# Kernel optimization log

Hardware: AMD Instinct MI355X
Metric: run time of the kernel (lower is better)

## Reference

```python
import jax, jax.numpy as jnp
import numpy as np

N = 7        # num_nodes
H = 128      # hidden_dim
F_IN = 32    # input_dim
LN_EPS = 1e-5
ALPHA = 0.2  # leaky relu slope
NEG = -9e15  # masking constant from torch code


def _layernorm(x, g, b):
    m = jnp.mean(x, axis=-1, keepdims=True)
    v = jnp.var(x, axis=-1, keepdims=True)
    return (x - m) * jax.lax.rsqrt(v + LN_EPS) * g + b


def setup_inputs() -> dict:
    key = jax.random.key(0)
    ks = jax.random.split(key, 12)
    B, T = 32, 512
    x = jax.random.normal(ks[0], (B, T, F_IN), dtype=jnp.float32)
    adj = jnp.ones((N, N), dtype=jnp.float32)
    # xavier-uniform style init scales (values don't matter for correctness test)
    def xav(k, shape, gain=1.414):
        fan_in, fan_out = shape[0], shape[-1]
        a = gain * np.sqrt(6.0 / (fan_in + fan_out))
        return jax.random.uniform(k, shape, jnp.float32, -a, a)
    Wp = xav(ks[1], (F_IN, N * H), gain=1.0)
    bp = jnp.zeros((N * H,), jnp.float32)
    W1 = xav(ks[2], (H, H))
    a1 = xav(ks[3], (2 * H, 1))
    g1 = jnp.ones((H,), jnp.float32)
    b1 = jnp.zeros((H,), jnp.float32)
    W2 = xav(ks[4], (H, H))
    a2 = xav(ks[5], (2 * H, 1))
    g2 = jnp.ones((H,), jnp.float32)
    b2 = jnp.zeros((H,), jnp.float32)
    return {"x": x, "adj": adj, "Wp": Wp, "bp": bp,
            "W1": W1, "a1": a1, "g1": g1, "b1": b1,
            "W2": W2, "a2": a2, "g2": g2, "b2": b2}


def reference(x, adj, Wp, bp, W1, a1, g1, b1, W2, a2, g2, b2):
    B, T, F = x.shape
    BT = B * T
    # input projection: (B*T, F) -> (B*T, N, H)
    h = (x.reshape(BT, F) @ Wp + bp).reshape(BT, N, H)
    scale = H ** (-0.5)
    mask = adj > 0  # (N, N)
    for (W, a, g, b) in ((W1, a1, g1, b1), (W2, a2, g2, b2)):
        res = h
        Wh = h @ W                               # (BT, N, H)
        # e_ij = leakyrelu(Wh_i . a[:H] + Wh_j . a[H:]) * scale
        f_src = Wh @ a[:H, 0]                    # (BT, N)
        f_dst = Wh @ a[H:, 0]                    # (BT, N)
        e = jax.nn.leaky_relu(f_src[:, :, None] + f_dst[:, None, :], ALPHA) * scale
        e = jnp.where(mask[None, :, :], e, NEG)
        att = jax.nn.softmax(e, axis=2)          # (BT, N, N)
        h_prime = att @ Wh                       # (BT, N, H), concat=False -> no elu
        h = _layernorm(h_prime, g, b) + res
    out = h.mean(axis=1)                         # mean over nodes
    return out.reshape(B, T, H)
```

## Files before the change

kernel.cpp:

```cpp
#include <hip/hip_runtime.h>
#include <math.h>
#include <stdint.h>

#define NN 7
#define HD 128
#define FIN 32
#define TPB 16
#define RPW 28
#define LN_EPS 1e-5f
#define ALPHA 0.2f
#define NEG_CONST -9e15f
#define SCALE 0.08838834764831845f

typedef __bf16 bf16x8 __attribute__((ext_vector_type(8)));
typedef float  f32x4  __attribute__((ext_vector_type(4)));

#define FENCE() do { asm volatile("s_waitcnt lgkmcnt(0)" ::: "memory"); \
                     __builtin_amdgcn_sched_barrier(0); } while (0)

__device__ __forceinline__ uint16_t f2bf_u(float f) {
    union { float f; uint32_t u; } v; v.f = f;
    uint32_t r = v.u + 0x7FFFu + ((v.u >> 16) & 1u);
    return (uint16_t)(r >> 16);
}
__device__ __forceinline__ uint32_t pack2(float a, float b) {
    return (uint32_t)f2bf_u(a) | ((uint32_t)f2bf_u(b) << 16);
}

template <int CTRL>
__device__ __forceinline__ float dpp_add(float v) {
    union { float f; int i; } a, r;
    a.f = v;
    r.i = __builtin_amdgcn_update_dpp(a.i, a.i, CTRL, 0xF, 0xF, false);
    return v + r.f;
}
__device__ __forceinline__ float sum16(float v) {
    v = dpp_add<0xB1>(v);
    v = dpp_add<0x4E>(v);
    v = dpp_add<0x124>(v);
    v = dpp_add<0x128>(v);
    return v;
}

#define WS_W1T  57344
#define WS_W2T  90112
#define WS_VAB  122880
#define WS_BPP  124928
#define WS_GBP  128512

__global__ __launch_bounds__(256) void prep_weights(
    const float* __restrict__ Wp, const float* __restrict__ bp,
    const float* __restrict__ W1, const float* __restrict__ a1,
    const float* __restrict__ g1, const float* __restrict__ b1,
    const float* __restrict__ W2, const float* __restrict__ a2,
    const float* __restrict__ g2, const float* __restrict__ b2,
    uint16_t* __restrict__ WpT, uint16_t* __restrict__ W1T,
    uint16_t* __restrict__ W2T, float* __restrict__ vab,
    float* __restrict__ bpp, float* __restrict__ gbp)
{
    const int bid = blockIdx.x, tid = threadIdx.x;
    if (bid < 112) {
        int idx = bid * 256 + tid;
        int gc = idx >> 5, f = idx & 31;
        int gcp = (gc & ~127) | (((gc & 15) << 3) | ((gc & 127) >> 4));
        WpT[gcp * 32 + f] = f2bf_u(Wp[(size_t)f * (NN * HD) + gc]);
    } else if (bid < 176) {
        int idx = (bid - 112) * 256 + tid;
        int c = idx >> 7, k = idx & 127;
        int kp = ((k & 15) << 3) | (k >> 4);
        W1T[c * 128 + kp] = f2bf_u(W1[(size_t)k * HD + c]);
    } else if (bid < 240) {
        int idx = (bid - 176) * 256 + tid;
        int c = idx >> 7, k = idx & 127;
        int kp = ((k & 15) << 3) | (k >> 4);
        W2T[c * 128 + kp] = f2bf_u(W2[(size_t)k * HD + c]);
    } else {
        for (int d = tid; d < 512; d += 256) {
            int l = d >> 8, which = (d >> 7) & 1, j = d & 127;
            const float* W = l ? W2 : W1;
            const float* a = (l ? a2 : a1) + which * HD;
            const float* row = W + (size_t)j * HD;
            float acc = 0.f;
            #pragma unroll 8
            for (int o = 0; o < HD; o += 4) {
                f32x4 wv = *reinterpret_cast<const f32x4*>(&row[o]);
                acc += wv[0]*a[o] + wv[1]*a[o+1] + wv[2]*a[o+2] + wv[3]*a[o+3];
            }
            int jp = ((j & 15) << 3) | (j >> 4);
            vab[l * 256 + which * 128 + jp] = acc;
        }
        for (int gc = tid; gc < NN * HD; gc += 256) {
            int gcp = (gc & ~127) | (((gc & 15) << 3) | ((gc & 127) >> 4));
            bpp[gcp] = bp[gc];
        }
        for (int e = tid; e < 512; e += 256) {
            int l = e >> 8, which = (e >> 7) & 1, c = e & 127;
            const float* src = l ? (which ? b2 : g2) : (which ? b1 : g1);
            int cp = ((c & 15) << 3) | (c >> 4);
            gbp[l * 256 + which * 128 + cp] = src[c];
        }
    }
}

__global__ __launch_bounds__(256, 2) void gat_fused(
    const float* __restrict__ x, const float* __restrict__ adj,
    const float* __restrict__ bpp,
    const uint16_t* __restrict__ WpT, const uint16_t* __restrict__ W1T,
    const uint16_t* __restrict__ W2T, const float* __restrict__ vab,
    const float* __restrict__ gbp,
    float* __restrict__ out, int BT)
{
    __shared__ __align__(16) float h_s[4][RPW][132];

    const int tid  = threadIdx.x;
    const int lane = tid & 63;
    const int wave = tid >> 6;
    const int frow = lane & 15;
    const int kgrp = lane >> 4;
    const int kb   = kgrp * 8;
    const int t0   = blockIdx.x * TPB;

    const int row0 = (frow > 13) ? 13 : frow;
    const int tb   = (row0 >= NN) ? 1 : 0;
    const int np   = row0 - tb * NN;

    uint32_t amask = 0;
    #pragma unroll
    for (int j = 0; j < NN; ++j)
        amask |= (adj[np * NN + j] > 0.f) ? (1u << j) : 0u;

    bf16x8 bx;
    {
        union { bf16x8 v; uint32_t u[4]; } bu;
        bu.u[0] = bu.u[1] = bu.u[2] = bu.u[3] = 0;
        int tok = t0 + frow;
        if (tok < BT) {
            f32x4 xa = *reinterpret_cast<const f32x4*>(&x[(size_t)tok * FIN + kb]);
            f32x4 xb = *reinterpret_cast<const f32x4*>(&x[(size_t)tok * FIN + kb + 4]);
            bu.u[0] = pack2(xa[0], xa[1]);
            bu.u[1] = pack2(xa[2], xa[3]);
            bu.u[2] = pack2(xb[0], xb[1]);
            bu.u[3] = pack2(xb[2], xb[3]);
        }
        bx = bu.v;
    }

    #pragma unroll 2
    for (int i = 0; i < 14; ++i) {
        int tile = wave * 14 + i;
        bf16x8 av = *reinterpret_cast<const bf16x8*>(WpT + (size_t)(tile * 16 + frow) * FIN + kb);
        f32x4 acc = {0.f, 0.f, 0.f, 0.f};
        acc = __builtin_amdgcn_mfma_f32_16x16x32_bf16(av, bx, acc, 0, 0, 0);
        int tok = t0 + frow;
        if (tok < BT) {
            int gc0 = tile * 16 + kgrp * 4;
            f32x4 bias = *reinterpret_cast<const f32x4*>(&bpp[gc0]);
            f32x4 v = acc + bias;
            int n = gc0 >> 7, kk = gc0 & 127;
            *reinterpret_cast<f32x4*>(&h_s[frow >> 2][(frow & 3) * NN + n][kk]) = v;
        }
    }
    __syncthreads();

    for (int l = 0; l < 2; ++l) {
        const uint16_t* __restrict__ WT  = l ? W2T : W1T;
        const float*    __restrict__ vv0 = vab + l * 256;
        const float*    __restrict__ ggp = gbp + l * 256;

        float facc;
        {
            int which = lane >> 5;
            int rr = lane & 31; if (rr > RPW - 1) rr = RPW - 1;
            const float* hr = &h_s[wave][rr][0];
            const f32x4* vp = reinterpret_cast<const f32x4*>(vv0 + which * HD);
            f32x4 a0 = {0,0,0,0}, a1 = {0,0,0,0};
            #pragma unroll
            for (int i2 = 0; i2 < 16; ++i2) {
                f32x4 hv0 = *reinterpret_cast<const f32x4*>(hr + i2 * 8);
                f32x4 hv1 = *reinterpret_cast<const f32x4*>(hr + i2 * 8 + 4);
                a0 += hv0 * vp[2 * i2];
                a1 += hv1 * vp[2 * i2 + 1];
            }
            f32x4 a = a0 + a1;
            facc = (a[0] + a[1]) + (a[2] + a[3]);
        }

        float p0[NN], p1[NN];
        {
            float fs0 = __shfl(facc, row0, 64);
            float fs1 = __shfl(facc, 14 + row0, 64);
            float e0[NN], e1[NN];
            float mx0 = -INFINITY, mx1 = -INFINITY;
            #pragma unroll
            for (int j = 0; j < NN; ++j) {
                float fd0 = __shfl(facc, 32 + tb * NN + j, 64);
                float fd1 = __shfl(facc, 32 + 14 + tb * NN + j, 64);
                float v0 = fs0 + fd0, v1 = fs1 + fd1;
                v0 = (v0 > 0.f ? v0 : ALPHA * v0) * SCALE;
                v1 = (v1 > 0.f ? v1 : ALPHA * v1) * SCALE;
                bool ok = (amask >> j) & 1u;
                v0 = ok ? v0 : NEG_CONST;
                v1 = ok ? v1 : NEG_CONST;
                e0[j] = v0; mx0 = fmaxf(mx0, v0);
                e1[j] = v1; mx1 = fmaxf(mx1, v1);
            }
            float s0 = 0.f, s1 = 0.f;
            #pragma unroll
            for (int j = 0; j < NN; ++j) {
                e0[j] = __expf(e0[j] - mx0); s0 += e0[j];
                e1[j] = __expf(e1[j] - mx1); s1 += e1[j];
            }
            float i0 = 1.f / s0, i1 = 1.f / s1;
            #pragma unroll
            for (int j = 0; j < NN; ++j) { p0[j] = e0[j] * i0; p1[j] = e1[j] * i1; }
        }

        bf16x8 avA[4], avB[4];
        #pragma unroll
        for (int ks = 0; ks < 4; ++ks) {
            f32x4 ga0 = {0,0,0,0}, ga1 = {0,0,0,0};
            f32x4 gb0 = {0,0,0,0}, gb1 = {0,0,0,0};
            #pragma unroll
            for (int j = 0; j < NN; ++j) {
                const float* hj = &h_s[wave][tb * NN + j][ks * 32 + kb];
                f32x4 h0 = *reinterpret_cast<const f32x4*>(hj);
                f32x4 h1 = *reinterpret_cast<const f32x4*>(hj + 4);
                float pj = p0[j];
                ga0 += h0 * pj;
                ga1 += h1 * pj;
            }
            #pragma unroll
            for (int j = 0; j < NN; ++j) {
                const float* hj = &h_s[wave][14 + tb * NN + j][ks * 32 + kb];
                f32x4 h0 = *reinterpret_cast<const f32x4*>(hj);
                f32x4 h1 = *reinterpret_cast<const f32x4*>(hj + 4);
                float pj = p1[j];
                gb0 += h0 * pj;
                gb1 += h1 * pj;
            }
            union { bf16x8 v; uint32_t u[4]; } ba, bb;
            ba.u[0] = pack2(ga0[0], ga0[1]); ba.u[1] = pack2(ga0[2], ga0[3]);
            ba.u[2] = pack2(ga1[0], ga1[1]); ba.u[3] = pack2(ga1[2], ga1[3]);
            bb.u[0] = pack2(gb0[0], gb0[1]); bb.u[1] = pack2(gb0[2], gb0[3]);
            bb.u[2] = pack2(gb1[0], gb1[1]); bb.u[3] = pack2(gb1[2], gb1[3]);
            avA[ks] = ba.v; avB[ks] = bb.v;
        }

        f32x4 C0[8], C1[8];
        #pragma unroll
        for (int ntl = 0; ntl < 8; ++ntl) {
            const uint16_t* bpg = WT + (size_t)(ntl * 16 + frow) * HD + kb;
            bf16x8 bv0 = *reinterpret_cast<const bf16x8*>(bpg);
            bf16x8 bv1 = *reinterpret_cast<const bf16x8*>(bpg + 32);
            bf16x8 bv2 = *reinterpret_cast<const bf16x8*>(bpg + 64);
            bf16x8 bv3 = *reinterpret_cast<const bf16x8*>(bpg + 96);
            f32x4 a0 = {0,0,0,0}, a1 = {0,0,0,0};
            a0 = __builtin_amdgcn_mfma_f32_16x16x32_bf16(avA[0], bv0, a0, 0, 0, 0);
            a1 = __builtin_amdgcn_mfma_f32_16x16x32_bf16(avB[0], bv0, a1, 0, 0, 0);
            a0 = __builtin_amdgcn_mfma_f32_16x16x32_bf16(avA[1], bv1, a0, 0, 0, 0);
            a1 = __builtin_amdgcn_mfma_f32_16x16x32_bf16(avB[1], bv1, a1, 0, 0, 0);
            a0 = __builtin_amdgcn_mfma_f32_16x16x32_bf16(avA[2], bv2, a0, 0, 0, 0);
            a1 = __builtin_amdgcn_mfma_f32_16x16x32_bf16(avB[2], bv2, a1, 0, 0, 0);
            a0 = __builtin_amdgcn_mfma_f32_16x16x32_bf16(avA[3], bv3, a0, 0, 0, 0);
            a1 = __builtin_amdgcn_mfma_f32_16x16x32_bf16(avB[3], bv3, a1, 0, 0, 0);
            C0[ntl] = a0; C1[ntl] = a1;
        }

        {
            f32x4 gv0 = *reinterpret_cast<const f32x4*>(ggp + frow * 8);
            f32x4 gv1 = *reinterpret_cast<const f32x4*>(ggp + frow * 8 + 4);
            f32x4 bt0 = *reinterpret_cast<const f32x4*>(ggp + 128 + frow * 8);
            f32x4 bt1 = *reinterpret_cast<const f32x4*>(ggp + 128 + frow * 8 + 4);
            #pragma unroll
            for (int tile = 0; tile < 2; ++tile) {
                const f32x4* C = tile ? C1 : C0;
                const int mbase = tile * 14;
                f32x4 s4 = C[0] + C[1];
                f32x4 q4 = C[0]*C[0] + C[1]*C[1];
                #pragma unroll
                for (int nt = 2; nt < 8; ++nt) { s4 += C[nt]; q4 += C[nt]*C[nt]; }
                #pragma unroll
                for (int r = 0; r < 4; ++r) {
                    float s  = sum16(s4[r]);
                    float sq = sum16(q4[r]);
                    float mean = s * (1.f / HD);
                    float var  = sq * (1.f / HD) - mean * mean;
                    float rinv = rsqrtf(var + LN_EPS);
                    int m = kgrp * 4 + r;
                    if (m < 14) {
                        f32x4 coef0 = gv0 * rinv, coef1 = gv1 * rinv;
                        f32x4 off0  = bt0 - coef0 * mean;
                        f32x4 off1  = bt1 - coef1 * mean;
                        float* hp = &h_s[wave][mbase + m][frow * 8];
                        f32x4 h0 = *reinterpret_cast<const f32x4*>(hp) + off0;
                        f32x4 h1 = *reinterpret_cast<const f32x4*>(hp + 4) + off1;
                        h0[0] += C[0][r] * coef0[0];
                        h0[1] += C[1][r] * coef0[1];
                        h0[2] += C[2][r] * coef0[2];
                        h0[3] += C[3][r] * coef0[3];
                        h1[0] += C[4][r] * coef1[0];
                        h1[1] += C[5][r] * coef1[1];
                        h1[2] += C[6][r] * coef1[2];
                        h1[3] += C[7][r] * coef1[3];
                        *reinterpret_cast<f32x4*>(hp)     = h0;
                        *reinterpret_cast<f32x4*>(hp + 4) = h1;
                    }
                }
            }
        }
        FENCE();
    }

    {
        int t_o = lane >> 4;
        int cq  = lane & 15;
        int tok = t0 + wave * 4 + t_o;
        if (tok < BT) {
            f32x4 s0 = {0,0,0,0}, s1 = {0,0,0,0};
            #pragma unroll
            for (int n = 0; n < NN; ++n) {
                const float* hp = &h_s[wave][t_o * NN + n][cq * 8];
                s0 += *reinterpret_cast<const f32x4*>(hp);
                s1 += *reinterpret_cast<const f32x4*>(hp + 4);
            }
            const float inv7 = 1.f / 7.f;
            s0 *= inv7; s1 *= inv7;
            float* ob = out + (size_t)tok * HD;
            ob[0*16+cq] = s0[0]; ob[1*16+cq] = s0[1];
            ob[2*16+cq] = s0[2]; ob[3*16+cq] = s0[3];
            ob[4*16+cq] = s1[0]; ob[5*16+cq] = s1[1];
            ob[6*16+cq] = s1[2]; ob[7*16+cq] = s1[3];
        }
    }
}

extern "C" void kernel_launch(void* const* d_in, const int* in_sizes, int n_in,
                              void* d_out, int out_size, void* d_ws, size_t ws_size,
                              hipStream_t stream) {
    const float* x   = (const float*)d_in[0];
    const float* adj = (const float*)d_in[1];
    const float* Wp  = (const float*)d_in[2];
    const float* bp  = (const float*)d_in[3];
    const float* W1  = (const float*)d_in[4];
    const float* a1  = (const float*)d_in[5];
    const float* g1  = (const float*)d_in[6];
    const float* b1  = (const float*)d_in[7];
    const float* W2  = (const float*)d_in[8];
    const float* a2  = (const float*)d_in[9];
    const float* g2  = (const float*)d_in[10];
    const float* b2  = (const float*)d_in[11];
    const int BT = in_sizes[0] / FIN;
    const int blocks = (BT + TPB - 1) / TPB;

    uint8_t* ws = (uint8_t*)d_ws;
    uint16_t* WpT = (uint16_t*)(ws);
    uint16_t* W1T = (uint16_t*)(ws + WS_W1T);
    uint16_t* W2T = (uint16_t*)(ws + WS_W2T);
    float*    vab = (float*)   (ws + WS_VAB);
    float*    bpp = (float*)   (ws + WS_BPP);
    float*    gbp = (float*)   (ws + WS_GBP);

    prep_weights<<<dim3(241), dim3(256), 0, stream>>>(
        Wp, bp, W1, a1, g1, b1, W2, a2, g2, b2, WpT, W1T, W2T, vab, bpp, gbp);
    gat_fused<<<dim3(blocks), dim3(256), 0, stream>>>(
        x, adj, bpp, WpT, W1T, W2T, vab, gbp, (float*)d_out, BT);
}
```

Measured before the change: 74.86 us.

## Store hidden state in LDS as bf16 and raise occupancy target to 4 blocks

The per-block shared hidden-state buffer changes from fp32 to packed bf16, with unpack helpers at every read and bf16 packing at every write, including the residual/LayerNorm update. This halves LDS footprint and LDS read bandwidth per row, and the launch bound is raised from 2 to 4 blocks per CU to use the freed LDS for more resident waves. The cost is extra pack/unpack ALU work, bf16 rounding of the residual stream across both layers (an accuracy risk), and tighter register limits that may cause spills.

```diff
diff --git a/kernel.cpp b/kernel.cpp
--- a/kernel.cpp
+++ b/kernel.cpp
@@ -25,6 +25,18 @@
 }
 __device__ __forceinline__ uint32_t pack2(float a, float b) {
     return (uint32_t)f2bf_u(a) | ((uint32_t)f2bf_u(b) << 16);
+}
+__device__ __forceinline__ float bflo(uint32_t u) {
+    union { uint32_t q; float f; } v; v.q = u << 16; return v.f;
+}
+__device__ __forceinline__ float bfhi(uint32_t u) {
+    union { uint32_t q; float f; } v; v.q = u & 0xffff0000u; return v.f;
+}
+__device__ __forceinline__ f32x4 unpk_lo(uint4 h) {
+    return (f32x4){bflo(h.x), bfhi(h.x), bflo(h.y), bfhi(h.y)};
+}
+__device__ __forceinline__ f32x4 unpk_hi(uint4 h) {
+    return (f32x4){bflo(h.z), bfhi(h.z), bflo(h.w), bfhi(h.w)};
 }
 
 template <int CTRL>
@@ -102,7 +114,7 @@
     }
 }
 
-__global__ __launch_bounds__(256, 2) void gat_fused(
+__global__ __launch_bounds__(256, 4) void gat_fused(
     const float* __restrict__ x, const float* __restrict__ adj,
     const float* __restrict__ bpp,
     const uint16_t* __restrict__ WpT, const uint16_t* __restrict__ W1T,
@@ -110,7 +122,7 @@
     const float* __restrict__ gbp,
     float* __restrict__ out, int BT)
 {
-    __shared__ __align__(16) float h_s[4][RPW][132];
+    __shared__ __align__(16) uint16_t h_s[4][RPW][136];
 
     const int tid  = threadIdx.x;
     const int lane = tid & 63;
@@ -157,7 +169,8 @@
             f32x4 bias = *reinterpret_cast<const f32x4*>(&bpp[gc0]);
             f32x4 v = acc + bias;
             int n = gc0 >> 7, kk = gc0 & 127;
-            *reinterpret_cast<f32x4*>(&h_s[frow >> 2][(frow & 3) * NN + n][kk]) = v;
+            uint2 uu = { pack2(v[0], v[1]), pack2(v[2], v[3]) };
+            *reinterpret_cast<uint2*>(&h_s[frow >> 2][(frow & 3) * NN + n][kk]) = uu;
         }
     }
     __syncthreads();
@@ -171,15 +184,14 @@
         {
             int which = lane >> 5;
             int rr = lane & 31; if (rr > RPW - 1) rr = RPW - 1;
-            const float* hr = &h_s[wave][rr][0];
+            const uint32_t* hr = reinterpret_cast<const uint32_t*>(&h_s[wave][rr][0]);
             const f32x4* vp = reinterpret_cast<const f32x4*>(vv0 + which * HD);
             f32x4 a0 = {0,0,0,0}, a1 = {0,0,0,0};
             #pragma unroll
             for (int i2 = 0; i2 < 16; ++i2) {
-                f32x4 hv0 = *reinterpret_cast<const f32x4*>(hr + i2 * 8);
-                f32x4 hv1 = *reinterpret_cast<const f32x4*>(hr + i2 * 8 + 4);
-                a0 += hv0 * vp[2 * i2];
-                a1 += hv1 * vp[2 * i2 + 1];
+                uint4 hv = *reinterpret_cast<const uint4*>(hr + i2 * 4);
+                a0 += unpk_lo(hv) * vp[2 * i2];
+                a1 += unpk_hi(hv) * vp[2 * i2 + 1];
             }
             f32x4 a = a0 + a1;
             facc = (a[0] + a[1]) + (a[2] + a[3]);
@@ -222,21 +234,17 @@
             f32x4 gb0 = {0,0,0,0}, gb1 = {0,0,0,0};
             #pragma unroll
             for (int j = 0; j < NN; ++j) {
-                const float* hj = &h_s[wave][tb * NN + j][ks * 32 + kb];
-                f32x4 h0 = *reinterpret_cast<const f32x4*>(hj);
-                f32x4 h1 = *reinterpret_cast<const f32x4*>(hj + 4);
+                uint4 hv = *reinterpret_cast<const uint4*>(&h_s[wave][tb * NN + j][ks * 32 + kb]);
                 float pj = p0[j];
-                ga0 += h0 * pj;
-                ga1 += h1 * pj;
+                ga0 += unpk_lo(hv) * pj;
+                ga1 += unpk_hi(hv) * pj;
             }
             #pragma unroll
             for (int j = 0; j < NN; ++j) {
-                const float* hj = &h_s[wave][14 + tb * NN + j][ks * 32 + kb];
-                f32x4 h0 = *reinterpret_cast<const f32x4*>(hj);
-                f32x4 h1 = *reinterpret_cast<const f32x4*>(hj + 4);
+                uint4 hv = *reinterpret_cast<const uint4*>(&h_s[wave][14 + tb * NN + j][ks * 32 + kb]);
                 float pj = p1[j];
-                gb0 += h0 * pj;
-                gb1 += h1 * pj;
+                gb0 += unpk_lo(hv) * pj;
+                gb1 += unpk_hi(hv) * pj;
             }
             union { bf16x8 v; uint32_t u[4]; } ba, bb;
             ba.u[0] = pack2(ga0[0], ga0[1]); ba.u[1] = pack2(ga0[2], ga0[3]);
@@ -291,9 +299,10 @@
                         f32x4 coef0 = gv0 * rinv, coef1 = gv1 * rinv;
                         f32x4 off0  = bt0 - coef0 * mean;
                         f32x4 off1  = bt1 - coef1 * mean;
-                        float* hp = &h_s[wave][mbase + m][frow * 8];
-                        f32x4 h0 = *reinterpret_cast<const f32x4*>(hp) + off0;
-                        f32x4 h1 = *reinterpret_cast<const f32x4*>(hp + 4) + off1;
+                        uint16_t* hp = &h_s[wave][mbase + m][frow * 8];
+                        uint4 hold = *reinterpret_cast<const uint4*>(hp);
+                        f32x4 h0 = unpk_lo(hold) + off0;
+                        f32x4 h1 = unpk_hi(hold) + off1;
                         h0[0] += C[0][r] * coef0[0];
                         h0[1] += C[1][r] * coef0[1];
                         h0[2] += C[2][r] * coef0[2];
@@ -302,8 +311,10 @@
                         h1[1] += C[5][r] * coef1[1];
                         h1[2] += C[6][r] * coef1[2];
                         h1[3] += C[7][r] * coef1[3];
-                        *reinterpret_cast<f32x4*>(hp)     = h0;
-                        *reinterpret_cast<f32x4*>(hp + 4) = h1;
+                        uint4 w;
+                        w.x = pack2(h0[0], h0[1]); w.y = pack2(h0[2], h0[3]);
+                        w.z = pack2(h1[0], h1[1]); w.w = pack2(h1[2], h1[3]);
+                        *reinterpret_cast<uint4*>(hp) = w;
                     }
                 }
             }
@@ -319,9 +330,9 @@
             f32x4 s0 = {0,0,0,0}, s1 = {0,0,0,0};
             #pragma unroll
             for (int n = 0; n < NN; ++n) {
-                const float* hp = &h_s[wave][t_o * NN + n][cq * 8];
-                s0 += *reinterpret_cast<const f32x4*>(hp);
-                s1 += *reinterpret_cast<const f32x4*>(hp + 4);
+                uint4 hv = *reinterpret_cast<const uint4*>(&h_s[wave][t_o * NN + n][cq * 8]);
+                s0 += unpk_lo(hv);
+                s1 += unpk_hi(hv);
             }
             const float inv7 = 1.f / 7.f;
             s0 *= inv7; s1 *= inv7;
```

New measurement: 83.35 us. 11.3% more time.
